# Optimization experiments

Measured on AMD Instinct MI355X. Metric: run time of the kernel, lower is better.

Reference implementation:

```python
import jax, jax.numpy as jnp
import numpy as np

K = 3          # kernel size
SH, SW = 2, 1  # stride
PH, PW = 1, 1  # padding


def conv2d(x, w, b, stride, pad):
    y = jax.lax.conv_general_dilated(
        x, w, window_strides=stride,
        padding=[(pad[0], pad[0]), (pad[1], pad[1])],
        dimension_numbers=('NCHW', 'OIHW', 'NCHW'))
    return y + b[None, :, None, None]


def setup_inputs() -> dict:
    key = jax.random.key(0)
    ks = jax.random.split(key, 4)
    x = jax.random.normal(ks[0], (8, 64, 128, 128), jnp.float32)
    # scale offset weights small so sampled offsets are O(1) pixels (exercises
    # the bilinear path without sampling far out of bounds)
    w_offset = jax.random.normal(ks[1], (18, 64, 3, 3), jnp.float32) * 0.02
    b_offset = jnp.zeros((18,), jnp.float32)
    w_mask = jax.random.normal(ks[2], (9, 64, 3, 3), jnp.float32) * 0.05
    b_mask = jnp.zeros((9,), jnp.float32)
    w_conv = jax.random.normal(ks[3], (64, 64, 3, 3), jnp.float32) * (1.0 / 24.0)
    return dict(x=x, w_offset=w_offset, b_offset=b_offset,
                w_mask=w_mask, b_mask=b_mask, w_conv=w_conv)


def _bilinear_gather(x, py, px):
    # x: [B,C,H,W]; py, px: [B,K2,Ho,Wo] float sampling coordinates.
    # Zero-padding outside the image (torchvision deform_conv2d semantics).
    B, C, H, W = x.shape
    y0f = jnp.floor(py)
    x0f = jnp.floor(px)
    dy = py - y0f
    dx = px - x0f
    y0 = y0f.astype(jnp.int32)
    x0 = x0f.astype(jnp.int32)

    def corner(yi, xi, wgt):
        valid = (yi >= 0) & (yi < H) & (xi >= 0) & (xi < W)
        yc = jnp.clip(yi, 0, H - 1)
        xc = jnp.clip(xi, 0, W - 1)
        # per-batch fancy gather -> [B, C, K2, Ho, Wo]
        g = jax.vmap(lambda xb, yb, xbi: xb[:, yb, xbi])(x, yc, xc)
        return g * (wgt * valid)[:, None]

    return (corner(y0,     x0,     (1 - dy) * (1 - dx))
            + corner(y0,     x0 + 1, (1 - dy) * dx)
            + corner(y0 + 1, x0,     dy * (1 - dx))
            + corner(y0 + 1, x0 + 1, dy * dx))


def reference(x, w_offset, b_offset, w_mask, b_mask, w_conv):
    B, C, H, W = x.shape
    offset = conv2d(x, w_offset, b_offset, (SH, SW), (PH, PW))   # [B, 2*K2, Ho, Wo]
    mask = jax.nn.sigmoid(conv2d(x, w_mask, b_mask, (SH, SW), (PH, PW)))  # [B, K2, Ho, Wo]
    Ho, Wo = offset.shape[2], offset.shape[3]
    K2 = K * K
    off = offset.reshape(B, K2, 2, Ho, Wo)
    off_y = off[:, :, 0]   # [B,K2,Ho,Wo]
    off_x = off[:, :, 1]
    ky = (jnp.arange(K2) // K).astype(jnp.float32)
    kx = (jnp.arange(K2) % K).astype(jnp.float32)
    hs = (jnp.arange(Ho) * SH - PH).astype(jnp.float32)
    ws = (jnp.arange(Wo) * SW - PW).astype(jnp.float32)
    py = off_y + ky[None, :, None, None] + hs[None, None, :, None]
    px = off_x + kx[None, :, None, None] + ws[None, None, None, :]
    sampled = _bilinear_gather(x, py, px) * mask[:, None]  # [B,C,K2,Ho,Wo]
    # weighted accumulate over in-channels and kernel taps
    out = jnp.einsum('ock,bckhw->bohw', w_conv.reshape(-1, C, K2), sampled)
    return out
```

## Files before the change

kernel.cpp:

```cpp
#include <hip/hip_runtime.h>
#include <hip/hip_fp16.h>
#include <math.h>

#define BB 8
#define CC 64
#define HH 128
#define WW 128
#define HO 64
#define WO 128
#define OC 64
#define HW (HH * WW)

typedef __attribute__((ext_vector_type(4))) float floatx4;
typedef __attribute__((ext_vector_type(8))) _Float16 half8;

__device__ __forceinline__ unsigned short f2h(float f) {
    __half h = __float2half(f);
    return __builtin_bit_cast(unsigned short, h);
}
__device__ __forceinline__ unsigned int packpair(float a, float b) {
    __half2 h = __floats2half2_rn(a, b);
    return __builtin_bit_cast(unsigned int, h);
}
__device__ __forceinline__ void lgkm_barrier() {
    asm volatile("s_waitcnt lgkmcnt(0)" ::: "memory");
    __builtin_amdgcn_s_barrier();
}

__global__ __launch_bounds__(256) void prep(
    const float* __restrict__ x,
    const float* __restrict__ w_off, const float* __restrict__ w_msk,
    const float* __restrict__ w_conv,
    unsigned int* __restrict__ xP,
    unsigned short* __restrict__ Wom, unsigned short* __restrict__ W2)
{
    __shared__ float T[66][65];
    int tid = threadIdx.x, bx = blockIdx.x;
    if (bx < 2048) {
        int wh = bx & 1, b = (bx >> 1) & 7, y = bx >> 4;
        int w0 = wh << 6;
        const float* xb = x + (((size_t)b * CC) * HH + y) * WW + w0;
#pragma unroll
        for (int i = 0; i < 4; ++i) {
            int idx = i * 256 + tid;
            int cch = idx >> 4, f4 = (idx & 15) << 2;
            floatx4 v = *(const floatx4*)(xb + (size_t)cch * HW + f4);
            T[f4 + 0][cch] = v.x;
            T[f4 + 1][cch] = v.y;
            T[f4 + 2][cch] = v.z;
            T[f4 + 3][cch] = v.w;
        }
        if (tid < 64) {
            float e = 0.0f;
            if (w0 + 64 < WW) e = xb[(size_t)tid * HW + 64];
            T[64][tid] = e;
        }
        __syncthreads();
        int c4 = tid & 15;
        int wr = tid >> 4;
        size_t rowbase = (((size_t)b * HH + y) * WW) + w0;
#pragma unroll
        for (int j = 0; j < 4; ++j) {
            int w = 16 * j + wr;
            floatx4 a  = *(const floatx4*)&T[w][4 * c4];
            floatx4 bb = *(const floatx4*)&T[w + 1][4 * c4];
            uint4 d;
            d.x = packpair(a.x, bb.x);
            d.y = packpair(a.y, bb.y);
            d.z = packpair(a.z, bb.z);
            d.w = packpair(a.w, bb.w);
            *(uint4*)(xP + (rowbase + w) * 64 + 4 * c4) = d;
        }
    } else if (bx < 2120) {
        int i = (bx - 2048) * 256 + tid;
        int chn = i / 576, kk = i % 576;
        int xs = kk >> 6, cc = kk & 63;
        float v = 0.0f;
        if (chn < 18)      v = w_off[(chn * CC + cc) * 9 + xs];
        else if (chn < 27) v = w_msk[((chn - 18) * CC + cc) * 9 + xs];
        Wom[i] = f2h(v);
    } else {
        int i = (bx - 2120) * 256 + tid;
        int k = i % 9, cc = (i / 9) % CC, o = i / (CC * 9);
        W2[((size_t)k * OC + o) * CC + cc] = f2h(w_conv[i]);
    }
}

__global__ __launch_bounds__(256, 2) void fused(
    const unsigned int* __restrict__ xP,
    const unsigned short* __restrict__ Wom, const unsigned short* __restrict__ W2,
    const float* __restrict__ b_off, const float* __restrict__ b_msk,
    float* __restrict__ out)
{
    __shared__ __align__(16) char lds[35968];
    _Float16* XsH = (_Float16*)lds;
    float* omr = (float*)(lds + 28544);
    uint2* metaR = (uint2*)lds;
    uint2* metaC = (uint2*)(lds + 4608);

    int tid = threadIdx.x;
    int lane = tid & 63;
    int wv = __builtin_amdgcn_readfirstlane(tid >> 6);
    int bx = blockIdx.x;
    int b = bx & 7;
    int rest = bx >> 3;
    int h = rest >> 1;
    int w0 = (rest & 1) << 6;
    int h2 = 2 * h - 1;
    int m16 = lane & 15, q = lane >> 4;

    const unsigned int* xPb_u = xP + (size_t)b * HW * 64;

    for (int u = tid; u < 3168; u += 256) {
        int ky = u / 1056;
        int rem = u - ky * 1056;
        int col = rem >> 4, c4 = rem & 15;
        int hy = h2 + ky, wc = w0 - 1 + col;
        unsigned int lo0 = 0u, lo1 = 0u;
        if ((unsigned)hy < (unsigned)HH && (unsigned)wc < (unsigned)WW) {
            const uint4 g = *(const uint4*)(xPb_u + ((size_t)hy * WW + wc) * 64 + c4 * 4);
            lo0 = (g.x & 0xffffu) | (g.y << 16);
            lo1 = (g.z & 0xffffu) | (g.w << 16);
        }
        *(uint2*)(XsH + (ky * 66 + col) * 72 + c4 * 4) = make_uint2(lo0, lo1);
    }
    lgkm_barrier();

    {
        int nt = wv;
        floatx4 a0 = (floatx4){0.f, 0.f, 0.f, 0.f};
        floatx4 a1 = (floatx4){0.f, 0.f, 0.f, 0.f};
        const _Float16* wa0 = (const _Float16*)Wom + m16 * 576 + q * 8;
        const _Float16* wa1 = wa0 + 16 * 576;
#pragma unroll
        for (int t = 0; t < 18; ++t) {
            int xs = t >> 1, ky = xs / 3, kx = xs % 3;
            half8 bf = *(const half8*)(XsH + (ky * 66 + nt * 16 + m16 + kx) * 72
                                       + (t & 1) * 32 + q * 8);
            half8 af0 = *(const half8*)(wa0 + t * 32);
            half8 af1 = *(const half8*)(wa1 + t * 32);
            a0 = __builtin_amdgcn_mfma_f32_16x16x32_f16(af0, bf, a0, 0, 0, 0);
            a1 = __builtin_amdgcn_mfma_f32_16x16x32_f16(af1, bf, a1, 0, 0, 0);
        }
#pragma unroll
        for (int r = 0; r < 4; ++r) {
            int c0 = q * 4 + r;
            omr[c0 * 68 + nt * 16 + m16] = a0[r];
            if (c0 + 16 < 27) omr[(c0 + 16) * 68 + nt * 16 + m16] = a1[r];
        }
    }
    lgkm_barrier();

    for (int u = tid; u < 576; u += 256) {
        int kk = u >> 6, pos = u & 63;
        float offy = omr[(2 * kk) * 68 + pos] + b_off[2 * kk];
        float offx = omr[(2 * kk + 1) * 68 + pos] + b_off[2 * kk + 1];
        float mk = 1.0f / (1.0f + __expf(-(omr[(18 + kk) * 68 + pos] + b_msk[kk])));
        float py = offy + (float)(kk / 3) + (float)h2;
        float px = offx + (float)(kk % 3) + (float)(w0 + pos - 1);

        float y0f = floorf(py), x0f = floorf(px);
        float dy = py - y0f, dx = px - x0f;
        int y0 = (int)y0f, x0 = (int)x0f;
        int y1 = y0 + 1, x1 = x0 + 1;
        bool vy0 = (unsigned)y0 < (unsigned)HH;
        bool vy1 = (unsigned)y1 < (unsigned)HH;
        bool vx0 = (unsigned)x0 < (unsigned)WW;
        bool vx1 = (unsigned)x1 < (unsigned)WW;
        float w00 = (1.0f - dy) * (1.0f - dx) * ((vy0 && vx0) ? mk : 0.0f);
        float w01 = (1.0f - dy) * dx          * ((vy0 && vx1) ? mk : 0.0f);
        float w10 = dy * (1.0f - dx)          * ((vy1 && vx0) ? mk : 0.0f);
        float w11 = dy * dx                   * ((vy1 && vx1) ? mk : 0.0f);
        int xbase = min(max(x0, 0), WW - 2);
        bool s0 = x0 > xbase;
        bool s1 = x1 > xbase;
        float cxA = (s0 ? 0.f : w00) + (s1 ? 0.f : w01);
        float cyA = (s0 ? w00 : 0.f) + (s1 ? w01 : 0.f);
        float cxB = (s0 ? 0.f : w10) + (s1 ? 0.f : w11);
        float cyB = (s0 ? w10 : 0.f) + (s1 ? w11 : 0.f);
        int yc0 = min(max(y0, 0), HH - 1);
        int yc1 = min(max(y1, 0), HH - 1);

        __half2 hA = __floats2half2_rn(cxA, cyA);
        __half2 hB = __floats2half2_rn(cxB, cyB);
        metaC[u] = make_uint2(__builtin_bit_cast(unsigned int, hA),
                              __builtin_bit_cast(unsigned int, hB));
        metaR[u] = make_uint2((unsigned)(yc0 * WW + xbase) * 256u,
                              (unsigned)(yc1 * WW + xbase) * 256u);
    }
    lgkm_barrier();

    int pw0 = wv * 16;
    int p = lane & 31;
    int ph = lane >> 5;
    unsigned int voffC = 8u * (unsigned)p;
    const char* xPb = (const char*)xPb_u;
    char* Sw = lds + 9216 + wv * 2048;

    floatx4 acc[4];
#pragma unroll
    for (int m = 0; m < 4; ++m) acc[m] = (floatx4){0.f, 0.f, 0.f, 0.f};

    half8 A[8];
    uint2 G0[8], G1[8];

    auto loadA = [&](int k) {
#pragma unroll
        for (int m = 0; m < 4; ++m)
#pragma unroll
            for (int ks = 0; ks < 2; ++ks)
                A[m * 2 + ks] = *(const half8*)((const _Float16*)W2
                    + ((size_t)(k * OC + m * 16 + m16)) * CC + ks * 32 + q * 8);
    };
    auto issueG = [&](int k) {
#pragma unroll
        for (int i = 0; i < 8; ++i) {
            uint2 zw = metaR[k * 64 + pw0 + ph * 8 + i];
            G0[i] = *(const uint2*)(xPb + (zw.x + voffC));
            G1[i] = *(const uint2*)(xPb + (zw.y + voffC));
        }
    };
    auto blend = [&](int k) {
#pragma unroll
        for (int i = 0; i < 8; ++i) {
            int rw = ph * 8 + i;
            uint2 cf = metaC[k * 64 + pw0 + rw];
            __half2 hA = __builtin_bit_cast(__half2, cf.x);
            __half2 hB = __builtin_bit_cast(__half2, cf.y);
            __half2 t0 = __hfma2(hA, __builtin_bit_cast(__half2, G0[i].x),
                                 __hmul2(hB, __builtin_bit_cast(__half2, G1[i].x)));
            __half2 t1 = __hfma2(hA, __builtin_bit_cast(__half2, G0[i].y),
                                 __hmul2(hB, __builtin_bit_cast(__half2, G1[i].y)));
            __half v0 = __hadd(__low2half(t0), __high2half(t0));
            __half v1 = __hadd(__low2half(t1), __high2half(t1));
            unsigned int d = (unsigned int)__builtin_bit_cast(unsigned short, v0)
                           | ((unsigned int)__builtin_bit_cast(unsigned short, v1) << 16);
            int cbi = p >> 2;
            *(unsigned int*)(Sw + rw * 128 + ((cbi ^ (rw & 7)) * 16 + (p & 3) * 4)) = d;
        }
    };
    auto mfma_tap = [&]() {
        half8 Bf[2];
#pragma unroll
        for (int ks = 0; ks < 2; ++ks) {
            int cbi = ks * 4 + q;
            Bf[ks] = *(const half8*)(Sw + m16 * 128 + ((cbi ^ (m16 & 7)) * 16));
        }
#pragma unroll
        for (int m = 0; m < 4; ++m)
#pragma unroll
            for (int ks = 0; ks < 2; ++ks)
                acc[m] = __builtin_amdgcn_mfma_f32_16x16x32_f16(A[m * 2 + ks], Bf[ks],
                                                                acc[m], 0, 0, 0);
    };

    loadA(0);
    issueG(0);
#pragma unroll 1
    for (int k = 0; k < 9; ++k) {
        blend(k);
        if (k < 8) issueG(k + 1);
        mfma_tap();
        if (k < 8) loadA(k + 1);
    }

#pragma unroll
    for (int m = 0; m < 4; ++m)
#pragma unroll
        for (int r = 0; r < 4; ++r) {
            int o = m * 16 + q * 4 + r;
            out[(((size_t)b * OC + o) * HO + h) * WO + w0 + pw0 + m16] = acc[m][r];
        }
}

extern "C" void kernel_launch(void* const* d_in, const int* in_sizes, int n_in,
                              void* d_out, int out_size, void* d_ws, size_t ws_size,
                              hipStream_t stream)
{
    const float* x      = (const float*)d_in[0];
    const float* w_off  = (const float*)d_in[1];
    const float* b_off  = (const float*)d_in[2];
    const float* w_msk  = (const float*)d_in[3];
    const float* b_msk  = (const float*)d_in[4];
    const float* w_conv = (const float*)d_in[5];
    float* out = (float*)d_out;

    unsigned int* xP = (unsigned int*)d_ws;
    unsigned short* Wom = (unsigned short*)(xP + (size_t)BB * HW * 64);
    unsigned short* W2 = Wom + 32 * 576;

    prep<<<dim3(2264), dim3(256), 0, stream>>>(x, w_off, w_msk, w_conv,
                                               xP, Wom, W2);
    fused<<<dim3(1024), dim3(256), 0, stream>>>(xP, Wom, W2,
                                                b_off, b_msk, out);
}
```

Measured before the change: 166.2 us.

## Make each wave own an independent 16-pixel tile, removing block barriers

Each wave now handles its own 16-output-pixel strip with a private LDS region, so the halo load, offset/mask MFMA and metadata stages need only a wave-local lgkmcnt wait instead of block-wide barriers. The gather loop is split into half-tap steps with double-buffered register sets so the next gathers are issued before the current blend. The occupancy hint is dropped from launch bounds. Per-wave halo loads now re-read overlapping columns (18 vs 66 per 64 pixels), adding some redundant global and LDS traffic.

```diff
diff --git a/kernel.cpp b/kernel.cpp
--- a/kernel.cpp
+++ b/kernel.cpp
@@ -22,9 +22,8 @@
     __half2 h = __floats2half2_rn(a, b);
     return __builtin_bit_cast(unsigned int, h);
 }
-__device__ __forceinline__ void lgkm_barrier() {
+__device__ __forceinline__ void wave_fence() {
     asm volatile("s_waitcnt lgkmcnt(0)" ::: "memory");
-    __builtin_amdgcn_s_barrier();
 }
 
 __global__ __launch_bounds__(256) void prep(
@@ -86,48 +85,49 @@
     }
 }
 
-__global__ __launch_bounds__(256, 2) void fused(
+__global__ __launch_bounds__(256) void fused(
     const unsigned int* __restrict__ xP,
     const unsigned short* __restrict__ Wom, const unsigned short* __restrict__ W2,
     const float* __restrict__ b_off, const float* __restrict__ b_msk,
     float* __restrict__ out)
 {
-    __shared__ __align__(16) char lds[35968];
-    _Float16* XsH = (_Float16*)lds;
-    float* omr = (float*)(lds + 28544);
-    uint2* metaR = (uint2*)lds;
-    uint2* metaC = (uint2*)(lds + 4608);
-
+    __shared__ __align__(16) char lds[38912];
     int tid = threadIdx.x;
     int lane = tid & 63;
     int wv = __builtin_amdgcn_readfirstlane(tid >> 6);
-    int bx = blockIdx.x;
-    int b = bx & 7;
-    int rest = bx >> 3;
-    int h = rest >> 1;
-    int w0 = (rest & 1) << 6;
+    char* wb = lds + wv * 9728;
+    _Float16* XsH = (_Float16*)wb;
+    float* omr = (float*)(wb + 7776);
+    uint2* metaRw = (uint2*)wb;
+    uint2* metaCw = (uint2*)(wb + 1152);
+    char* Sw = wb + 2304;
+
+    int g = blockIdx.x * 4 + wv;
+    int b = g >> 9;
+    int rem = g & 511;
+    int h = rem >> 3;
+    int w0 = (rem & 7) << 4;
     int h2 = 2 * h - 1;
     int m16 = lane & 15, q = lane >> 4;
 
     const unsigned int* xPb_u = xP + (size_t)b * HW * 64;
 
-    for (int u = tid; u < 3168; u += 256) {
-        int ky = u / 1056;
-        int rem = u - ky * 1056;
-        int col = rem >> 4, c4 = rem & 15;
+    for (int u = lane; u < 864; u += 64) {
+        int ky = u / 288;
+        int rm = u - ky * 288;
+        int col = rm >> 4, c4 = rm & 15;
         int hy = h2 + ky, wc = w0 - 1 + col;
         unsigned int lo0 = 0u, lo1 = 0u;
         if ((unsigned)hy < (unsigned)HH && (unsigned)wc < (unsigned)WW) {
-            const uint4 g = *(const uint4*)(xPb_u + ((size_t)hy * WW + wc) * 64 + c4 * 4);
-            lo0 = (g.x & 0xffffu) | (g.y << 16);
-            lo1 = (g.z & 0xffffu) | (g.w << 16);
-        }
-        *(uint2*)(XsH + (ky * 66 + col) * 72 + c4 * 4) = make_uint2(lo0, lo1);
-    }
-    lgkm_barrier();
+            const uint4 gg = *(const uint4*)(xPb_u + ((size_t)hy * WW + wc) * 64 + c4 * 4);
+            lo0 = (gg.x & 0xffffu) | (gg.y << 16);
+            lo1 = (gg.z & 0xffffu) | (gg.w << 16);
+        }
+        *(uint2*)(XsH + (ky * 18 + col) * 72 + c4 * 4) = make_uint2(lo0, lo1);
+    }
+    wave_fence();
 
     {
-        int nt = wv;
         floatx4 a0 = (floatx4){0.f, 0.f, 0.f, 0.f};
         floatx4 a1 = (floatx4){0.f, 0.f, 0.f, 0.f};
         const _Float16* wa0 = (const _Float16*)Wom + m16 * 576 + q * 8;
@@ -135,7 +135,7 @@
 #pragma unroll
         for (int t = 0; t < 18; ++t) {
             int xs = t >> 1, ky = xs / 3, kx = xs % 3;
-            half8 bf = *(const half8*)(XsH + (ky * 66 + nt * 16 + m16 + kx) * 72
+            half8 bf = *(const half8*)(XsH + (ky * 18 + m16 + kx) * 72
                                        + (t & 1) * 32 + q * 8);
             half8 af0 = *(const half8*)(wa0 + t * 32);
             half8 af1 = *(const half8*)(wa1 + t * 32);
@@ -145,17 +145,17 @@
 #pragma unroll
         for (int r = 0; r < 4; ++r) {
             int c0 = q * 4 + r;
-            omr[c0 * 68 + nt * 16 + m16] = a0[r];
-            if (c0 + 16 < 27) omr[(c0 + 16) * 68 + nt * 16 + m16] = a1[r];
-        }
-    }
-    lgkm_barrier();
-
-    for (int u = tid; u < 576; u += 256) {
-        int kk = u >> 6, pos = u & 63;
-        float offy = omr[(2 * kk) * 68 + pos] + b_off[2 * kk];
-        float offx = omr[(2 * kk + 1) * 68 + pos] + b_off[2 * kk + 1];
-        float mk = 1.0f / (1.0f + __expf(-(omr[(18 + kk) * 68 + pos] + b_msk[kk])));
+            omr[c0 * 17 + m16] = a0[r];
+            if (c0 + 16 < 27) omr[(c0 + 16) * 17 + m16] = a1[r];
+        }
+    }
+    wave_fence();
+
+    for (int u = lane; u < 144; u += 64) {
+        int kk = u >> 4, pos = u & 15;
+        float offy = omr[(2 * kk) * 17 + pos] + b_off[2 * kk];
+        float offx = omr[(2 * kk + 1) * 17 + pos] + b_off[2 * kk + 1];
+        float mk = 1.0f / (1.0f + __expf(-(omr[(18 + kk) * 17 + pos] + b_msk[kk])));
         float py = offy + (float)(kk / 3) + (float)h2;
         float px = offx + (float)(kk % 3) + (float)(w0 + pos - 1);
 
@@ -183,26 +183,24 @@
 
         __half2 hA = __floats2half2_rn(cxA, cyA);
         __half2 hB = __floats2half2_rn(cxB, cyB);
-        metaC[u] = make_uint2(__builtin_bit_cast(unsigned int, hA),
-                              __builtin_bit_cast(unsigned int, hB));
-        metaR[u] = make_uint2((unsigned)(yc0 * WW + xbase) * 256u,
-                              (unsigned)(yc1 * WW + xbase) * 256u);
-    }
-    lgkm_barrier();
-
-    int pw0 = wv * 16;
+        metaCw[u] = make_uint2(__builtin_bit_cast(unsigned int, hA),
+                               __builtin_bit_cast(unsigned int, hB));
+        metaRw[u] = make_uint2((unsigned)(yc0 * WW + xbase) * 256u,
+                               (unsigned)(yc1 * WW + xbase) * 256u);
+    }
+    wave_fence();
+
     int p = lane & 31;
-    int ph = lane >> 5;
+    int ph4 = (lane >> 5) << 2;
     unsigned int voffC = 8u * (unsigned)p;
     const char* xPb = (const char*)xPb_u;
-    char* Sw = lds + 9216 + wv * 2048;
 
     floatx4 acc[4];
 #pragma unroll
     for (int m = 0; m < 4; ++m) acc[m] = (floatx4){0.f, 0.f, 0.f, 0.f};
 
     half8 A[8];
-    uint2 G0[8], G1[8];
+    uint2 Ga0[4], Ga1[4], Gb0[4], Gb1[4];
 
     auto loadA = [&](int k) {
 #pragma unroll
@@ -212,19 +210,22 @@
                 A[m * 2 + ks] = *(const half8*)((const _Float16*)W2
                     + ((size_t)(k * OC + m * 16 + m16)) * CC + ks * 32 + q * 8);
     };
-    auto issueG = [&](int k) {
-#pragma unroll
-        for (int i = 0; i < 8; ++i) {
-            uint2 zw = metaR[k * 64 + pw0 + ph * 8 + i];
+    auto issueG = [&](int hhk, uint2 (&G0)[4], uint2 (&G1)[4]) {
+        int k = hhk >> 1;
+#pragma unroll
+        for (int i = 0; i < 4; ++i) {
+            int rw = ((hhk & 1) << 3) + ph4 + i;
+            uint2 zw = metaRw[k * 16 + rw];
             G0[i] = *(const uint2*)(xPb + (zw.x + voffC));
             G1[i] = *(const uint2*)(xPb + (zw.y + voffC));
         }
     };
-    auto blend = [&](int k) {
-#pragma unroll
-        for (int i = 0; i < 8; ++i) {
-            int rw = ph * 8 + i;
-            uint2 cf = metaC[k * 64 + pw0 + rw];
+    auto blend = [&](int hhk, uint2 (&G0)[4], uint2 (&G1)[4]) {
+        int k = hhk >> 1;
+#pragma unroll
+        for (int i = 0; i < 4; ++i) {
+            int rw = ((hhk & 1) << 3) + ph4 + i;
+            uint2 cf = metaCw[k * 16 + rw];
             __half2 hA = __builtin_bit_cast(__half2, cf.x);
             __half2 hB = __builtin_bit_cast(__half2, cf.y);
             __half2 t0 = __hfma2(hA, __builtin_bit_cast(__half2, G0[i].x),
@@ -235,33 +236,37 @@
             __half v1 = __hadd(__low2half(t1), __high2half(t1));
             unsigned int d = (unsigned int)__builtin_bit_cast(unsigned short, v0)
                            | ((unsigned int)__builtin_bit_cast(unsigned short, v1) << 16);
-            int cbi = p >> 2;
-            *(unsigned int*)(Sw + rw * 128 + ((cbi ^ (rw & 7)) * 16 + (p & 3) * 4)) = d;
+            *(unsigned int*)(Sw + rw * 128
+                + (((p >> 2) ^ (rw & 7)) * 16 + (p & 3) * 4)) = d;
         }
     };
     auto mfma_tap = [&]() {
-        half8 Bf[2];
-#pragma unroll
-        for (int ks = 0; ks < 2; ++ks) {
-            int cbi = ks * 4 + q;
-            Bf[ks] = *(const half8*)(Sw + m16 * 128 + ((cbi ^ (m16 & 7)) * 16));
-        }
-#pragma unroll
-        for (int m = 0; m < 4; ++m)
-#pragma unroll
-            for (int ks = 0; ks < 2; ++ks)
-                acc[m] = __builtin_amdgcn_mfma_f32_16x16x32_f16(A[m * 2 + ks], Bf[ks],
-                                                                acc[m], 0, 0, 0);
+        half8 Bf0 = *(const half8*)(Sw + m16 * 128 + ((q ^ (m16 & 7)) * 16));
+        half8 Bf1 = *(const half8*)(Sw + m16 * 128 + (((4 + q) ^ (m16 & 7)) * 16));
+#pragma unroll
+        for (int m = 0; m < 4; ++m) {
+            acc[m] = __builtin_amdgcn_mfma_f32_16x16x32_f16(A[m * 2 + 0], Bf0, acc[m], 0, 0, 0);
+            acc[m] = __builtin_amdgcn_mfma_f32_16x16x32_f16(A[m * 2 + 1], Bf1, acc[m], 0, 0, 0);
+        }
     };
 
     loadA(0);
-    issueG(0);
+    issueG(0, Ga0, Ga1);
 #pragma unroll 1
-    for (int k = 0; k < 9; ++k) {
-        blend(k);
-        if (k < 8) issueG(k + 1);
-        mfma_tap();
-        if (k < 8) loadA(k + 1);
+    for (int hh = 0; hh < 18; ++hh) {
+        if (hh < 17) {
+            if ((hh & 1) == 0) issueG(hh + 1, Gb0, Gb1);
+            else               issueG(hh + 1, Ga0, Ga1);
+        }
+        __builtin_amdgcn_sched_barrier(0);
+        if ((hh & 1) == 0) blend(hh, Ga0, Ga1);
+        else               blend(hh, Gb0, Gb1);
+        if (hh & 1) {
+            wave_fence();
+            mfma_tap();
+            if (hh < 17) loadA((hh >> 1) + 1);
+            __builtin_amdgcn_sched_barrier(0);
+        }
     }
 
 #pragma unroll
@@ -269,7 +274,7 @@
 #pragma unroll
         for (int r = 0; r < 4; ++r) {
             int o = m * 16 + q * 4 + r;
-            out[(((size_t)b * OC + o) * HO + h) * WO + w0 + pw0 + m16] = acc[m][r];
+            out[(((size_t)b * OC + o) * HO + h) * WO + w0 + m16] = acc[m][r];
         }
 }
 
```

New measurement: 168.1 us. Within noise of the previous version (+1.2%).
